# Kernel tuning notes

Hardware: AMD Instinct MI355X
Metric: run time of the kernel (lower is better)

The kernel has to match this reference:

```python
import jax, jax.numpy as jnp
import numpy as np

K_SIZE = 3
CH_IN = 256
NFILT = 256

def setup_inputs() -> dict:
    key = jax.random.key(0)
    k1, k2 = jax.random.split(key)
    x = jax.random.normal(k1, (32, 56, 56, CH_IN), dtype=jnp.float32)
    stdv = 1.0 / np.sqrt(K_SIZE * K_SIZE * CH_IN)
    w = jax.random.normal(k2, (K_SIZE, K_SIZE, CH_IN, NFILT), dtype=jnp.float32) * stdv
    pruning_mask = jnp.ones((K_SIZE * K_SIZE * CH_IN, NFILT), dtype=jnp.float32)
    return {"x": x, "w": w, "pruning_mask": pruning_mask}

def _magnitude_aware_weight(w):
    # scale = mean |w| over (kh, kw, cin), per output filter; stop-gradient
    scale = jax.lax.stop_gradient(jnp.mean(jnp.abs(w), axis=(0, 1, 2), keepdims=True))
    bw_no_grad = scale * jnp.sign(w)
    clipped = jnp.clip(w, -1.0, 1.0)
    # STE: forward = scale*sign(w), backward = d(clip(w,-1,1))
    return jax.lax.stop_gradient(bw_no_grad) - jax.lax.stop_gradient(clipped) + clipped

def reference(x, w, pruning_mask):
    kernel = _magnitude_aware_weight(w) * pruning_mask.reshape(K_SIZE, K_SIZE, CH_IN, NFILT)
    out = jax.lax.conv_general_dilated(
        x, kernel,
        window_strides=(1, 1),
        padding="SAME",
        dimension_numbers=("NHWC", "HWIO", "NHWC"),
    )
    return out
```

## Files before the change

### kernel.cpp

```cpp
#include <hip/hip_runtime.h>

typedef unsigned short u16;
typedef u16 u16x8 __attribute__((ext_vector_type(8)));
typedef __bf16 bf16x8 __attribute__((ext_vector_type(8)));
typedef float f32x4 __attribute__((ext_vector_type(4)));

#define NPIX 100352
#define KTOT 2304
#define IMG_PAD (58 * 58 * 256)

static __device__ __forceinline__ u16 f2bf(float f) {
  unsigned u = __float_as_uint(f);
  return (u16)((u + 0x7fffu + ((u >> 16) & 1u)) >> 16);
}

static __device__ __forceinline__ void gld_lds16(const u16* g, u16* l) {
  __builtin_amdgcn_global_load_lds(
      (const __attribute__((address_space(1))) void*)g,
      (__attribute__((address_space(3))) void*)l, 16, 0, 0);
}

__global__ void scale_accum_k(const float* __restrict__ w, float* __restrict__ scale) {
  const int t = threadIdx.x;
  const float* p = w + (long)blockIdx.x * 64 * 256 + t;
  float acc = 0.f;
#pragma unroll
  for (int e = 0; e < 64; ++e) acc += fabsf(p[(long)e * 256]);
  atomicAdd(&scale[t], acc);
}

__global__ void pack_w_k(const float* __restrict__ w, const float* __restrict__ mask,
                         const float* __restrict__ ssum, u16* __restrict__ wp) {
  __shared__ u16 t[128][33];
  const int k0 = blockIdx.x * 32;
  const int f0 = blockIdx.y * 128;
  const int tid = threadIdx.x;
#pragma unroll
  for (int i = 0; i < 16; ++i) {
    int idx = tid + i * 256;
    int kk = idx >> 7;
    int ff = idx & 127;
    long g = (long)(k0 + kk) * 256 + f0 + ff;
    float wv = w[g];
    float mv = mask[g];
    float sc = ssum[f0 + ff] * (1.0f / 2304.0f);
    float sg = (wv > 0.f) ? 1.f : ((wv < 0.f) ? -1.f : 0.f);
    t[ff][kk] = f2bf(sc * sg * mv);
  }
  __syncthreads();
#pragma unroll
  for (int i = 0; i < 8; ++i) {
    int idx = tid + i * 256;
    int row = idx >> 4;
    int c = idx & 15;
    unsigned v = (unsigned)t[row][2 * c] | ((unsigned)t[row][2 * c + 1] << 16);
    *(unsigned*)(wp + (long)(f0 + row) * KTOT + k0 + 2 * c) = v;
  }
}

__global__ void fill_xpad2_k(const float* __restrict__ x, u16* __restrict__ xp) {
  const long idx = (long)blockIdx.x * 256 + threadIdx.x;
  const int c = (int)(idx & 31);
  const long p = idx >> 5;
  const int img = (int)(p / 3364);
  const int r = (int)(p % 3364);
  const int ph = r / 58, pw = r % 58;
  u16x8 v = {0, 0, 0, 0, 0, 0, 0, 0};
  if (ph >= 1 && ph <= 56 && pw >= 1 && pw <= 56) {
    const float* s = x + ((long)img * 3136 + (ph - 1) * 56 + (pw - 1)) * 256 + c * 8;
    float4 a = *(const float4*)s;
    float4 b = *(const float4*)(s + 4);
    v[0] = f2bf(a.x); v[1] = f2bf(a.y); v[2] = f2bf(a.z); v[3] = f2bf(a.w);
    v[4] = f2bf(b.x); v[5] = f2bf(b.y); v[6] = f2bf(b.z); v[7] = f2bf(b.w);
  }
  *(u16x8*)(xp + idx * 8) = v;
}

__global__ __launch_bounds__(256) void conv_gemm4_k(
    const u16* __restrict__ xpad, const u16* __restrict__ wp, float* __restrict__ out) {
  __shared__ u16 As[128 * 64];
  __shared__ u16 Bs[128 * 64];

  const int tid = threadIdx.x;
  const int lane = tid & 63;
  const int wv = tid >> 6;
  const int m0 = blockIdx.x * 128;
  const int n0 = blockIdx.y * 128;

  const int lsub = lane >> 3;
  const int lc = (lane & 7) ^ (lsub & 7);
  const u16* aptr[4];
  const u16* bptr[4];
#pragma unroll
  for (int i = 0; i < 4; ++i) {
    const int row = (i * 4 + wv) * 8 + lsub;
    const int m = m0 + row;
    const int img = m / 3136, q = m % 3136;
    aptr[i] = xpad + (long)img * IMG_PAD + ((q / 56 + 1) * 58 + (q % 56) + 1) * 256 + lc * 8;
    bptr[i] = wp + (long)(n0 + row) * KTOT + lc * 8;
  }
  const int ldsb = wv * 512;

  const int lm = lane & 15, kq = lane >> 4;
  const int wm = wv & 1, wn = wv >> 1;
  int aoff[2], boff[2];
#pragma unroll
  for (int ct = 0; ct < 2; ++ct) {
    const int pc = ((ct * 4 + kq) ^ (lm & 7)) * 8;
    aoff[ct] = (wm * 64 + lm) * 64 + pc;
    boff[ct] = (wn * 64 + lm) * 64 + pc;
  }

  f32x4 acc[4][4] = {};

  for (int khw = 0; khw < 9; ++khw) {
    const int d = ((khw / 3 - 1) * 58 + (khw % 3 - 1)) * 256;
    const int bk = khw * 256;
#pragma unroll
    for (int j = 0; j < 4; ++j) {
      const int ka = d + j * 64;
      const int kb = bk + j * 64;
      __syncthreads();
#pragma unroll
      for (int i = 0; i < 4; ++i) {
        gld_lds16(aptr[i] + ka, As + i * 2048 + ldsb);
        gld_lds16(bptr[i] + kb, Bs + i * 2048 + ldsb);
      }
      __syncthreads();
#pragma unroll
      for (int ct = 0; ct < 2; ++ct) {
        bf16x8 av[4], bv[4];
#pragma unroll
        for (int mi = 0; mi < 4; ++mi) av[mi] = *(const bf16x8*)(As + aoff[ct] + mi * 1024);
#pragma unroll
        for (int ni = 0; ni < 4; ++ni) bv[ni] = *(const bf16x8*)(Bs + boff[ct] + ni * 1024);
#pragma unroll
        for (int mi = 0; mi < 4; ++mi)
#pragma unroll
          for (int ni = 0; ni < 4; ++ni)
            acc[mi][ni] = __builtin_amdgcn_mfma_f32_16x16x32_bf16(av[mi], bv[ni], acc[mi][ni], 0, 0, 0);
      }
    }
  }

  float* op = out + (long)(m0 + wm * 64 + kq * 4) * 256 + n0 + wn * 64 + lm;
#pragma unroll
  for (int mi = 0; mi < 4; ++mi) {
#pragma unroll
    for (int ni = 0; ni < 4; ++ni) {
      float* p = op + (long)mi * 16 * 256 + ni * 16;
      f32x4 v = acc[mi][ni];
      p[0] = v[0];
      p[256] = v[1];
      p[512] = v[2];
      p[768] = v[3];
    }
  }
}

__global__ __launch_bounds__(256) void conv_gemm_fb_k(
    const float* __restrict__ x, const u16* __restrict__ wp, float* __restrict__ out) {
  __shared__ u16 As[128 * 40];
  __shared__ u16 Bs[128 * 40];
  const int tid = threadIdx.x;
  const int m0 = blockIdx.x * 128;
  const int n0 = blockIdx.y * 128;
  const int cc = tid & 3;
  const int r0 = tid >> 2;
  const int gm0 = m0 + r0;
  const int gm1 = gm0 + 64;
  const int pix0 = gm0 % 3136, oh0 = pix0 / 56, ow0 = pix0 % 56;
  const int pix1 = gm1 % 3136, oh1 = pix1 / 56, ow1 = pix1 % 56;
  const int lane = tid & 63;
  const int wv = tid >> 6;
  const int wm = wv & 1, wn = wv >> 1;
  const int lm = lane & 15, kq = lane >> 4;
  const int aoff = (wm * 64 + lm) * 40 + kq * 8;
  const int boff = (wn * 64 + lm) * 40 + kq * 8;
  u16* as0 = As + r0 * 40 + cc * 8;
  u16* as1 = As + (r0 + 64) * 40 + cc * 8;
  u16* bs0 = Bs + r0 * 40 + cc * 8;
  u16* bs1 = Bs + (r0 + 64) * 40 + cc * 8;
  const u16* wr0 = wp + (long)(n0 + r0) * KTOT + cc * 8;
  const u16* wr1 = wr0 + (long)64 * KTOT;
  f32x4 acc[4][4] = {};
  for (int khw = 0; khw < 9; ++khw) {
    const int dh = khw / 3 - 1;
    const int dw = khw % 3 - 1;
    const bool v0 = ((unsigned)(oh0 + dh) < 56u) && ((unsigned)(ow0 + dw) < 56u);
    const bool v1 = ((unsigned)(oh1 + dh) < 56u) && ((unsigned)(ow1 + dw) < 56u);
    const long p0 = ((long)gm0 + dh * 56 + dw) * 256 + cc * 8;
    const long p1 = ((long)gm1 + dh * 56 + dw) * 256 + cc * 8;
    const u16* wk0 = wr0 + khw * 256;
    const u16* wk1 = wr1 + khw * 256;
    for (int ct = 0; ct < 8; ++ct) {
      const int ci0 = ct * 32;
      u16x8 a0 = {0,0,0,0,0,0,0,0}, a1 = {0,0,0,0,0,0,0,0};
      float4 l0 = make_float4(0,0,0,0), h0 = make_float4(0,0,0,0);
      float4 l1 = make_float4(0,0,0,0), h1 = make_float4(0,0,0,0);
      if (v0) { l0 = *(const float4*)(x + p0 + ci0); h0 = *(const float4*)(x + p0 + ci0 + 4); }
      if (v1) { l1 = *(const float4*)(x + p1 + ci0); h1 = *(const float4*)(x + p1 + ci0 + 4); }
      a0[0]=f2bf(l0.x); a0[1]=f2bf(l0.y); a0[2]=f2bf(l0.z); a0[3]=f2bf(l0.w);
      a0[4]=f2bf(h0.x); a0[5]=f2bf(h0.y); a0[6]=f2bf(h0.z); a0[7]=f2bf(h0.w);
      a1[0]=f2bf(l1.x); a1[1]=f2bf(l1.y); a1[2]=f2bf(l1.z); a1[3]=f2bf(l1.w);
      a1[4]=f2bf(h1.x); a1[5]=f2bf(h1.y); a1[6]=f2bf(h1.z); a1[7]=f2bf(h1.w);
      u16x8 b0 = *(const u16x8*)(wk0 + ci0);
      u16x8 b1 = *(const u16x8*)(wk1 + ci0);
      __syncthreads();
      *(u16x8*)as0 = a0; *(u16x8*)as1 = a1;
      *(u16x8*)bs0 = b0; *(u16x8*)bs1 = b1;
      __syncthreads();
      bf16x8 av[4], bv[4];
#pragma unroll
      for (int i = 0; i < 4; ++i) av[i] = *(const bf16x8*)(As + aoff + i * 640);
#pragma unroll
      for (int i = 0; i < 4; ++i) bv[i] = *(const bf16x8*)(Bs + boff + i * 640);
#pragma unroll
      for (int mi = 0; mi < 4; ++mi)
#pragma unroll
        for (int ni = 0; ni < 4; ++ni)
          acc[mi][ni] = __builtin_amdgcn_mfma_f32_16x16x32_bf16(av[mi], bv[ni], acc[mi][ni], 0, 0, 0);
    }
  }
  float* op = out + (long)(m0 + wm * 64 + kq * 4) * 256 + n0 + wn * 64 + lm;
#pragma unroll
  for (int mi = 0; mi < 4; ++mi)
#pragma unroll
    for (int ni = 0; ni < 4; ++ni) {
      float* p = op + (long)mi * 16 * 256 + ni * 16;
      f32x4 v = acc[mi][ni];
      p[0] = v[0]; p[256] = v[1]; p[512] = v[2]; p[768] = v[3];
    }
}

extern "C" void kernel_launch(void* const* d_in, const int* in_sizes, int n_in,
                              void* d_out, int out_size, void* d_ws, size_t ws_size,
                              hipStream_t stream) {
  const float* x = (const float*)d_in[0];
  const float* w = (const float*)d_in[1];
  const float* mask = (const float*)d_in[2];
  float* out = (float*)d_out;

  float* scale = (float*)d_ws;
  u16* wp = (u16*)((char*)d_ws + 1088);
  u16* xpad = (u16*)((char*)d_ws + 1088 + 1179648);
  const size_t xpad_bytes = (size_t)32 * IMG_PAD * 2;
  const size_t need = 1088 + 1179648 + xpad_bytes;

  hipMemsetAsync(d_ws, 0, 1088, stream);
  scale_accum_k<<<36, 256, 0, stream>>>(w, scale);
  pack_w_k<<<dim3(72, 2), 256, 0, stream>>>(w, mask, scale, wp);
  if (ws_size >= need) {
    fill_xpad2_k<<<(32 * 3364 * 32) / 256, 256, 0, stream>>>(x, xpad);
    conv_gemm4_k<<<dim3(784, 2), 256, 0, stream>>>(xpad, wp, out);
  } else {
    conv_gemm_fb_k<<<dim3(784, 2), 256, 0, stream>>>(x, wp, out);
  }
}
```

Measured before the change: 377.4 us.

## Double-buffer LDS tiles with async prefetch and swizzle block order

Converts the implicit-GEMM conv main loop to a two-stage LDS double buffer: the next K-tile is issued through global_load_lds while MFMAs run on the current tile, with explicit vmcnt waits and raw barriers in place of __syncthreads. The grid is also flattened to a 1D launch, and block IDs are remapped so that neighbouring blocks (presumably co-resident across XCDs) share A/B tiles in cache. The aim is to hide global load latency and improve L2 reuse. In exchange, LDS use doubles to 64KB per block, which may lower occupancy, and correctness now depends on the hand-counted vmcnt(8) value.

```diff
diff --git a/kernel.cpp b/kernel.cpp
--- a/kernel.cpp
+++ b/kernel.cpp
@@ -76,16 +76,19 @@
   *(u16x8*)(xp + idx * 8) = v;
 }
 
-__global__ __launch_bounds__(256) void conv_gemm4_k(
+__global__ __launch_bounds__(256) void conv_gemm5_k(
     const u16* __restrict__ xpad, const u16* __restrict__ wp, float* __restrict__ out) {
-  __shared__ u16 As[128 * 64];
-  __shared__ u16 Bs[128 * 64];
+  __shared__ u16 As[2][128 * 64];
+  __shared__ u16 Bs[2][128 * 64];
 
   const int tid = threadIdx.x;
   const int lane = tid & 63;
   const int wv = tid >> 6;
-  const int m0 = blockIdx.x * 128;
-  const int n0 = blockIdx.y * 128;
+
+  const int orig = blockIdx.x;
+  const int swz = (orig & 7) * 196 + (orig >> 3);
+  const int m0 = (swz >> 1) * 128;
+  const int n0 = (swz & 1) * 128;
 
   const int lsub = lane >> 3;
   const int lc = (lane & 7) ^ (lsub & 7);
@@ -113,34 +116,52 @@
 
   f32x4 acc[4][4] = {};
 
-  for (int khw = 0; khw < 9; ++khw) {
-    const int d = ((khw / 3 - 1) * 58 + (khw % 3 - 1)) * 256;
-    const int bk = khw * 256;
-#pragma unroll
-    for (int j = 0; j < 4; ++j) {
-      const int ka = d + j * 64;
-      const int kb = bk + j * 64;
-      __syncthreads();
+  {
+    const int ka = -59 * 256;
+#pragma unroll
+    for (int i = 0; i < 4; ++i) {
+      gld_lds16(aptr[i] + ka, As[0] + i * 2048 + ldsb);
+      gld_lds16(bptr[i], Bs[0] + i * 2048 + ldsb);
+    }
+  }
+
+  for (int kt = 0; kt < 36; ++kt) {
+    const int cur = kt & 1;
+    if (kt < 35) {
+      const int kn = kt + 1;
+      const int khw = kn >> 2;
+      const int d = ((khw / 3 - 1) * 58 + (khw % 3 - 1)) * 256;
+      const int ka = d + (kn & 3) * 64;
+      const int kb = kn * 64;
 #pragma unroll
       for (int i = 0; i < 4; ++i) {
-        gld_lds16(aptr[i] + ka, As + i * 2048 + ldsb);
-        gld_lds16(bptr[i] + kb, Bs + i * 2048 + ldsb);
+        gld_lds16(aptr[i] + ka, As[cur ^ 1] + i * 2048 + ldsb);
+        gld_lds16(bptr[i] + kb, Bs[cur ^ 1] + i * 2048 + ldsb);
       }
-      __syncthreads();
-#pragma unroll
-      for (int ct = 0; ct < 2; ++ct) {
-        bf16x8 av[4], bv[4];
-#pragma unroll
-        for (int mi = 0; mi < 4; ++mi) av[mi] = *(const bf16x8*)(As + aoff[ct] + mi * 1024);
-#pragma unroll
-        for (int ni = 0; ni < 4; ++ni) bv[ni] = *(const bf16x8*)(Bs + boff[ct] + ni * 1024);
-#pragma unroll
-        for (int mi = 0; mi < 4; ++mi)
-#pragma unroll
-          for (int ni = 0; ni < 4; ++ni)
-            acc[mi][ni] = __builtin_amdgcn_mfma_f32_16x16x32_bf16(av[mi], bv[ni], acc[mi][ni], 0, 0, 0);
-      }
-    }
+      asm volatile("s_waitcnt vmcnt(8)" ::: "memory");
+    } else {
+      asm volatile("s_waitcnt vmcnt(0)" ::: "memory");
+    }
+    __builtin_amdgcn_s_barrier();
+    asm volatile("" ::: "memory");
+
+#pragma unroll
+    for (int ct = 0; ct < 2; ++ct) {
+      bf16x8 av[4], bv[4];
+#pragma unroll
+      for (int mi = 0; mi < 4; ++mi) av[mi] = *(const bf16x8*)(As[cur] + aoff[ct] + mi * 1024);
+#pragma unroll
+      for (int ni = 0; ni < 4; ++ni) bv[ni] = *(const bf16x8*)(Bs[cur] + boff[ct] + ni * 1024);
+#pragma unroll
+      for (int mi = 0; mi < 4; ++mi)
+#pragma unroll
+        for (int ni = 0; ni < 4; ++ni)
+          acc[mi][ni] = __builtin_amdgcn_mfma_f32_16x16x32_bf16(av[mi], bv[ni], acc[mi][ni], 0, 0, 0);
+    }
+
+    asm volatile("" ::: "memory");
+    __builtin_amdgcn_s_barrier();
+    asm volatile("" ::: "memory");
   }
 
   float* op = out + (long)(m0 + wm * 64 + kq * 4) * 256 + n0 + wn * 64 + lm;
@@ -252,7 +273,7 @@
   pack_w_k<<<dim3(72, 2), 256, 0, stream>>>(w, mask, scale, wp);
   if (ws_size >= need) {
     fill_xpad2_k<<<(32 * 3364 * 32) / 256, 256, 0, stream>>>(x, xpad);
-    conv_gemm4_k<<<dim3(784, 2), 256, 0, stream>>>(xpad, wp, out);
+    conv_gemm5_k<<<1568, 256, 0, stream>>>(xpad, wp, out);
   } else {
     conv_gemm_fb_k<<<dim3(784, 2), 256, 0, stream>>>(x, wp, out);
   }
```

Result: no change. 374.6 us (-0.7%).
